# Kernel tuning notes

Measured on AMD Instinct MI355X. Metric: run time of the kernel, lower is better.

## Reference

```python
import jax, jax.numpy as jnp
import numpy as np

B, T, D, NH = 2, 2048, 1024, 32
HD = D // NH  # 32
EPS = 1e-6


def rms_norm(x):
    # normalize over head dim in fp32, cast back
    ms = jnp.mean(x.astype(jnp.float32) ** 2, axis=-1, keepdims=True)
    return x * jax.lax.rsqrt(ms + EPS).astype(x.dtype)


def apply_rope(x, cos, sin):
    d = x.shape[-1] // 2
    x1, x2 = x[..., :d], x[..., d:]
    c = cos[: x.shape[-2], :d]
    s = sin[: x.shape[-2], :d]
    return jnp.concatenate([x1 * c - x2 * s, x2 * c + x1 * s], axis=-1)


def setup_inputs() -> dict:
    key = jax.random.key(0)
    ks = jax.random.split(key, 5)
    sc = 1.0 / np.sqrt(D)
    x = jax.random.normal(ks[0], (B, T, D), jnp.float32)
    Wq = jax.random.normal(ks[1], (D, D), jnp.float32) * sc
    Wk = jax.random.normal(ks[2], (NH * HD, D), jnp.float32) * sc
    Wv = jax.random.normal(ks[3], (NH * HD, D), jnp.float32) * sc
    Wproj = jax.random.normal(ks[4], (D, D), jnp.float32) * sc
    q_gain = jnp.ones((NH,), jnp.float32)  # qk_gain = 1.0
    # real RoPE tables, shape [T, HD//2]
    pos = np.arange(T, dtype=np.float32)
    inv = 1.0 / (10000.0 ** (np.arange(HD // 2, dtype=np.float32) / (HD // 2)))
    ang = pos[:, None] * inv[None, :]
    cos = jnp.asarray(np.cos(ang), jnp.float32)
    sin = jnp.asarray(np.sin(ang), jnp.float32)
    return {"x": x, "Wq": Wq, "Wk": Wk, "Wv": Wv, "Wproj": Wproj,
            "q_gain": q_gain, "cos": cos, "sin": sin}


def reference(x, Wq, Wk, Wv, Wproj, q_gain, cos, sin):
    Bx, Tx, Dx = x.shape
    nh = q_gain.shape[0]
    hd = Dx // nh
    # projections -> [B, H, T, hd]
    q = (x @ Wq.T).reshape(Bx, Tx, nh, hd).transpose(0, 2, 1, 3)
    k = (x @ Wk.T).reshape(Bx, Tx, nh, hd).transpose(0, 2, 1, 3)
    v = (x @ Wv.T).reshape(Bx, Tx, nh, hd).transpose(0, 2, 1, 3)
    q = apply_rope(rms_norm(q), cos, sin) * q_gain[None, :, None, None]
    k = apply_rope(rms_norm(k), cos, sin)
    scale = hd ** (-0.5)
    scores = jnp.einsum('bhqd,bhkd->bhqk', q, k) * scale
    causal = jnp.tril(jnp.ones((Tx, Tx), bool))
    scores = jnp.where(causal, scores, jnp.finfo(scores.dtype).min)
    attn = jax.nn.softmax(scores, axis=-1)
    y = jnp.einsum('bhqk,bhkd->bhqd', attn, v)
    y = y.transpose(0, 2, 1, 3).reshape(Bx, Tx, Dx)
    return y @ Wproj.T
```

## Files before the change

kernel.cpp:

```cpp
#include <hip/hip_runtime.h>

#define DEV __device__ __forceinline__

typedef __bf16 bf16x8 __attribute__((ext_vector_type(8)));
typedef float f32x4 __attribute__((ext_vector_type(4)));
typedef float f32x16 __attribute__((ext_vector_type(16)));
typedef unsigned int u32x2 __attribute__((ext_vector_type(2)));

static constexpr int Tn = 2048;
static constexpr int Dn = 1024;
static constexpr int NHn = 32;
static constexpr int Mn = 2 * Tn;
static constexpr float QSCALE = 0.17677669529663687f * 1.4426950408889634f;

DEV unsigned short f2bf(float f) {
    return __builtin_bit_cast(unsigned short, (__bf16)f);
}

DEV unsigned pkbf(float lo, float hi) {
    unsigned short l = __builtin_bit_cast(unsigned short, (__bf16)lo);
    unsigned short h = __builtin_bit_cast(unsigned short, (__bf16)hi);
    return (unsigned)l | ((unsigned)h << 16);
}

#define GPTR(p) ((const __attribute__((address_space(1))) void*)(p))
#define LPTR(p) ((__attribute__((address_space(3))) void*)(p))

__global__ __launch_bounds__(256) void cast_all(
    const float* __restrict__ x, const float* __restrict__ Wq, const float* __restrict__ Wk,
    const float* __restrict__ Wv, const float* __restrict__ Wp,
    unsigned short* __restrict__ xb, unsigned short* __restrict__ wall) {
    int i = blockIdx.x * 256 + threadIdx.x;
    const float* src;
    ushort4* dst;
    if (i < (1 << 20)) {
        src = x + (size_t)i * 4;
        dst = reinterpret_cast<ushort4*>(xb) + i;
    } else {
        int j = i - (1 << 20);
        int sel = j >> 18, off = j & ((1 << 18) - 1);
        const float* w = (sel == 0) ? Wq : (sel == 1) ? Wk : (sel == 2) ? Wv : Wp;
        src = w + (size_t)off * 4;
        dst = reinterpret_cast<ushort4*>(wall) + ((size_t)sel << 18) + off;
    }
    float4 v = *reinterpret_cast<const float4*>(src);
    ushort4 o;
    o.x = f2bf(v.x); o.y = f2bf(v.y); o.z = f2bf(v.z); o.w = f2bf(v.w);
    *dst = o;
}

__global__ __launch_bounds__(256) void gemm_qkv(
    const unsigned short* __restrict__ A, const unsigned short* __restrict__ Wall,
    unsigned short* __restrict__ Qn, unsigned short* __restrict__ Kn, unsigned short* __restrict__ Vt,
    const float* __restrict__ gain, const float* __restrict__ cosp, const float* __restrict__ sinp) {
    const int z = blockIdx.z;
    const unsigned short* Bm = Wall + (size_t)z * (Dn * Dn);
    const int m0 = blockIdx.x * 128, n0 = blockIdx.y * 128;
    const int tid = threadIdx.x, w = tid >> 6, l = tid & 63;
    const int wm = w & 1, wn = w >> 1, lm = l & 15, quad = l >> 4;

    __shared__ __align__(16) unsigned short As[128 * 32];
    __shared__ __align__(16) unsigned short Bs[128 * 32];

    f32x4 acc[4][4] = {};

    const int r0 = (w * 2 + 0) * 16 + (l >> 2);
    const int r1 = (w * 2 + 1) * 16 + (l >> 2);
    const int c0 = (l & 3) * 8;
    const unsigned short* gA0 = A + (long)(m0 + r0) * Dn + c0;
    const unsigned short* gA1 = A + (long)(m0 + r1) * Dn + c0;
    const unsigned short* gB0 = Bm + (long)(n0 + r0) * Dn + c0;
    const unsigned short* gB1 = Bm + (long)(n0 + r1) * Dn + c0;
    unsigned short* lA0 = As + (w * 2 + 0) * 16 * 32;
    unsigned short* lA1 = As + (w * 2 + 1) * 16 * 32;
    unsigned short* lB0 = Bs + (w * 2 + 0) * 16 * 32;
    unsigned short* lB1 = Bs + (w * 2 + 1) * 16 * 32;

    for (int kk = 0; kk < Dn; kk += 32) {
        __builtin_amdgcn_global_load_lds(GPTR(gA0 + kk), LPTR(lA0), 16, 0, 0);
        __builtin_amdgcn_global_load_lds(GPTR(gA1 + kk), LPTR(lA1), 16, 0, 0);
        __builtin_amdgcn_global_load_lds(GPTR(gB0 + kk), LPTR(lB0), 16, 0, 0);
        __builtin_amdgcn_global_load_lds(GPTR(gB1 + kk), LPTR(lB1), 16, 0, 0);
        __syncthreads();
        bf16x8 af[4], bfv[4];
#pragma unroll
        for (int mt = 0; mt < 4; ++mt)
            af[mt] = __builtin_bit_cast(bf16x8,
                *reinterpret_cast<const uint4*>(As + (wm * 64 + mt * 16 + lm) * 32 + quad * 8));
#pragma unroll
        for (int nt = 0; nt < 4; ++nt)
            bfv[nt] = __builtin_bit_cast(bf16x8,
                *reinterpret_cast<const uint4*>(Bs + (wn * 64 + nt * 16 + lm) * 32 + quad * 8));
#pragma unroll
        for (int mt = 0; mt < 4; ++mt)
#pragma unroll
            for (int nt = 0; nt < 4; ++nt)
                acc[mt][nt] = __builtin_amdgcn_mfma_f32_16x16x32_bf16(af[mt], bfv[nt], acc[mt][nt], 0, 0, 0);
        __syncthreads();
    }

    if (z == 2) {
#pragma unroll
        for (int mt = 0; mt < 4; ++mt) {
            int row0 = m0 + wm * 64 + mt * 16 + quad * 4;
            int b_ = row0 >> 11, t_ = row0 & (Tn - 1);
#pragma unroll
            for (int nt = 0; nt < 4; ++nt) {
                int col = n0 + wn * 64 + nt * 16 + lm;
                int hh = col >> 5, dd = col & 31;
                ushort4 o4;
                o4.x = f2bf(acc[mt][nt][0]); o4.y = f2bf(acc[mt][nt][1]);
                o4.z = f2bf(acc[mt][nt][2]); o4.w = f2bf(acc[mt][nt][3]);
                *reinterpret_cast<ushort4*>(&Vt[((long)(b_ * NHn + hh) * 32 + dd) * Tn + t_]) = o4;
            }
        }
    } else {
        unsigned short* dst = z ? Kn : Qn;
#pragma unroll
        for (int mt = 0; mt < 4; ++mt)
#pragma unroll
            for (int r = 0; r < 4; ++r) {
                int row = m0 + wm * 64 + mt * 16 + quad * 4 + r;
                int b_ = row >> 11, t_ = row & (Tn - 1);
                float c = cosp[t_ * 16 + lm], s = sinp[t_ * 16 + lm];
#pragma unroll
                for (int g = 0; g < 2; ++g) {
                    float x1 = acc[mt][2 * g][r], x2 = acc[mt][2 * g + 1][r];
                    float ssv = x1 * x1 + x2 * x2;
#pragma unroll
                    for (int off = 8; off >= 1; off >>= 1) ssv += __shfl_xor(ssv, off, 16);
                    float rinv = rsqrtf(ssv * (1.0f / 32.0f) + 1e-6f);
                    x1 *= rinv; x2 *= rinv;
                    float o1 = x1 * c - x2 * s;
                    float o2 = x2 * c + x1 * s;
                    int hh = (n0 + wn * 64 + g * 32) >> 5;
                    if (z == 0) { float gs = gain[hh] * QSCALE; o1 *= gs; o2 *= gs; }
                    long base = ((long)(b_ * NHn + hh) * Tn + t_) * 32;
                    dst[base + lm] = f2bf(o1);
                    dst[base + 16 + lm] = f2bf(o2);
                }
            }
    }
}

__global__ __launch_bounds__(256) void gemm_proj(
    const unsigned short* __restrict__ A, const unsigned short* __restrict__ Bm,
    float* __restrict__ C) {
    const int m0 = blockIdx.x * 128, n0 = blockIdx.y * 128;
    const int tid = threadIdx.x, w = tid >> 6, l = tid & 63;
    const int wm = w & 1, wn = w >> 1, lm = l & 15, quad = l >> 4;

    __shared__ __align__(16) unsigned short As[128 * 32];
    __shared__ __align__(16) unsigned short Bs[128 * 32];

    f32x4 acc[4][4] = {};

    const int r0 = (w * 2 + 0) * 16 + (l >> 2);
    const int r1 = (w * 2 + 1) * 16 + (l >> 2);
    const int c0 = (l & 3) * 8;
    const unsigned short* gA0 = A + (long)(m0 + r0) * Dn + c0;
    const unsigned short* gA1 = A + (long)(m0 + r1) * Dn + c0;
    const unsigned short* gB0 = Bm + (long)(n0 + r0) * Dn + c0;
    const unsigned short* gB1 = Bm + (long)(n0 + r1) * Dn + c0;
    unsigned short* lA0 = As + (w * 2 + 0) * 16 * 32;
    unsigned short* lA1 = As + (w * 2 + 1) * 16 * 32;
    unsigned short* lB0 = Bs + (w * 2 + 0) * 16 * 32;
    unsigned short* lB1 = Bs + (w * 2 + 1) * 16 * 32;

    for (int kk = 0; kk < Dn; kk += 32) {
        __builtin_amdgcn_global_load_lds(GPTR(gA0 + kk), LPTR(lA0), 16, 0, 0);
        __builtin_amdgcn_global_load_lds(GPTR(gA1 + kk), LPTR(lA1), 16, 0, 0);
        __builtin_amdgcn_global_load_lds(GPTR(gB0 + kk), LPTR(lB0), 16, 0, 0);
        __builtin_amdgcn_global_load_lds(GPTR(gB1 + kk), LPTR(lB1), 16, 0, 0);
        __syncthreads();
        bf16x8 af[4], bfv[4];
#pragma unroll
        for (int mt = 0; mt < 4; ++mt)
            af[mt] = __builtin_bit_cast(bf16x8,
                *reinterpret_cast<const uint4*>(As + (wm * 64 + mt * 16 + lm) * 32 + quad * 8));
#pragma unroll
        for (int nt = 0; nt < 4; ++nt)
            bfv[nt] = __builtin_bit_cast(bf16x8,
                *reinterpret_cast<const uint4*>(Bs + (wn * 64 + nt * 16 + lm) * 32 + quad * 8));
#pragma unroll
        for (int mt = 0; mt < 4; ++mt)
#pragma unroll
            for (int nt = 0; nt < 4; ++nt)
                acc[mt][nt] = __builtin_amdgcn_mfma_f32_16x16x32_bf16(af[mt], bfv[nt], acc[mt][nt], 0, 0, 0);
        __syncthreads();
    }
#pragma unroll
    for (int mt = 0; mt < 4; ++mt)
#pragma unroll
        for (int nt = 0; nt < 4; ++nt)
#pragma unroll
            for (int r = 0; r < 4; ++r) {
                int rg = m0 + wm * 64 + mt * 16 + quad * 4 + r;
                int cg = n0 + wn * 64 + nt * 16 + lm;
                C[(long)rg * Dn + cg] = acc[mt][nt][r];
            }
}

__global__ __launch_bounds__(256) void attn(
    const unsigned short* __restrict__ Qn, const unsigned short* __restrict__ Kn,
    const unsigned short* __restrict__ Vt, unsigned short* __restrict__ Y) {
    const int bx = blockIdx.x, h = blockIdx.y, b = blockIdx.z;
    const int tid = threadIdx.x, w = tid >> 6, l = tid & 63;
    const int lr = l & 31, hf = l >> 5;
    const long bh = b * NHn + h;
    const unsigned short* Qh = Qn + bh * Tn * 32;
    const unsigned short* Kh = Kn + bh * Tn * 32;
    const unsigned short* Vh = Vt + bh * 32 * Tn;

    __shared__ __align__(16) unsigned short KT[2][2048];
    __shared__ __align__(16) unsigned short VT[2][2048];

    const int k_row = w * 16 + (l >> 2);
    const int k_s = ((l & 3) - (k_row >> 1)) & 3;
    const unsigned short* ksrc = Kh + k_row * 32 + k_s * 8;
    const int v_row = w * 8 + (l >> 3);
    const int v_s = ((l & 7) - v_row) & 7;
    const unsigned short* vsrc = Vh + (long)v_row * Tn + v_s * 8;

    for (int pass = 0; pass < 2; ++pass) {
        const int qb = pass ? (15 - bx) : bx;
        const int q0 = qb * 128 + w * 32;

        bf16x8 qf[2];
        qf[0] = __builtin_bit_cast(bf16x8,
            *reinterpret_cast<const uint4*>(Qh + (q0 + lr) * 32 + hf * 8));
        qf[1] = __builtin_bit_cast(bf16x8,
            *reinterpret_cast<const uint4*>(Qh + (q0 + lr) * 32 + 16 + hf * 8));
        float ss = 0.f;
#pragma unroll
        for (int j = 0; j < 8; ++j) {
            float v0 = (float)qf[0][j], v1 = (float)qf[1][j];
            ss += v0 * v0 + v1 * v1;
        }
        ss += __shfl_xor(ss, 32);
        const float Mv = __builtin_sqrtf(ss * 32.0f);
        f32x16 negC;
#pragma unroll
        for (int i = 0; i < 16; ++i) negC[i] = -Mv;

        float lsum = 0.f;
        f32x16 o = {};

        const int kend = q0 + 31;
        const int ntb = 2 * qb + 2;

        auto stage = [&](int buf, int k0) {
            __builtin_amdgcn_global_load_lds(GPTR(ksrc + k0 * 32), LPTR(&KT[buf][w * 512]), 16, 0, 0);
            __builtin_amdgcn_global_load_lds(GPTR(vsrc + k0), LPTR(&VT[buf][w * 512]), 16, 0, 0);
        };

        auto compute_t = [&](int buf, int k0) {
#pragma unroll
            for (int sub = 0; sub < 2; ++sub) {
                const int ks = k0 + sub * 32;
                if (ks > kend) continue;
                const int krow = sub * 32 + lr;
                const int sl0 = ((0 + hf) + (krow >> 1)) & 3;
                const int sl1 = ((2 + hf) + (krow >> 1)) & 3;
                bf16x8 k0f = __builtin_bit_cast(bf16x8,
                    *reinterpret_cast<const uint4*>(&KT[buf][krow * 32 + sl0 * 8]));
                bf16x8 k1f = __builtin_bit_cast(bf16x8,
                    *reinterpret_cast<const uint4*>(&KT[buf][krow * 32 + sl1 * 8]));
                f32x16 st = __builtin_amdgcn_mfma_f32_32x32x16_bf16(k0f, qf[0], negC, 0, 0, 0);
                st = __builtin_amdgcn_mfma_f32_32x32x16_bf16(k1f, qf[1], st, 0, 0, 0);
                const bool full = (ks + 31) <= q0;
                const int qrow = q0 + lr;
                float p[16];
#pragma unroll
                for (int r = 0; r < 16; ++r) {
                    float pv = __builtin_amdgcn_exp2f(st[r]);
                    if (!full) {
                        int kg = ks + (r & 3) + 8 * (r >> 2) + 4 * hf;
                        pv = (kg <= qrow) ? pv : 0.0f;
                    }
                    p[r] = pv;
                }
                float t0 = (p[0] + p[1]) + (p[2] + p[3]);
                float t1 = (p[4] + p[5]) + (p[6] + p[7]);
                float t2 = (p[8] + p[9]) + (p[10] + p[11]);
                float t3 = (p[12] + p[13]) + (p[14] + p[15]);
                lsum += (t0 + t1) + (t2 + t3);
                unsigned A0 = pkbf(p[0], p[1]), A1 = pkbf(p[2], p[3]);
                unsigned B0 = pkbf(p[4], p[5]), B1 = pkbf(p[6], p[7]);
                unsigned A2 = pkbf(p[8], p[9]), A3 = pkbf(p[10], p[11]);
                unsigned B2 = pkbf(p[12], p[13]), B3 = pkbf(p[14], p[15]);
                u32x2 s0 = __builtin_amdgcn_permlane32_swap(A0, B0, false, false);
                u32x2 s1 = __builtin_amdgcn_permlane32_swap(A1, B1, false, false);
                u32x2 s2 = __builtin_amdgcn_permlane32_swap(A2, B2, false, false);
                u32x2 s3 = __builtin_amdgcn_permlane32_swap(A3, B3, false, false);
                uint4 f0; f0.x = s0[0]; f0.y = s1[0]; f0.z = s0[1]; f0.w = s1[1];
                uint4 f1; f1.x = s2[0]; f1.y = s3[0]; f1.z = s2[1]; f1.w = s3[1];
                const int slv0 = ((sub * 4 + 0 + hf) + lr) & 7;
                const int slv1 = ((sub * 4 + 2 + hf) + lr) & 7;
                bf16x8 v0f = __builtin_bit_cast(bf16x8,
                    *reinterpret_cast<const uint4*>(&VT[buf][lr * 64 + slv0 * 8]));
                bf16x8 v1f = __builtin_bit_cast(bf16x8,
                    *reinterpret_cast<const uint4*>(&VT[buf][lr * 64 + slv1 * 8]));
                o = __builtin_amdgcn_mfma_f32_32x32x16_bf16(
                    __builtin_bit_cast(bf16x8, f0), v0f, o, 0, 0, 0);
                o = __builtin_amdgcn_mfma_f32_32x32x16_bf16(
                    __builtin_bit_cast(bf16x8, f1), v1f, o, 0, 0, 0);
            }
        };

        __syncthreads();
        stage(0, 0);
        int cur = 0;
        for (int ti = 0; ti < ntb; ++ti) {
            __syncthreads();
            if (ti + 1 < ntb) stage(cur ^ 1, (ti + 1) * 64);
            compute_t(cur, ti * 64);
            cur ^= 1;
        }

        lsum += __shfl_xor(lsum, 32);
        const float inv = 1.0f / lsum;
#pragma unroll
        for (int r = 0; r < 16; ++r) {
            int qr = (r & 3) + 8 * (r >> 2) + 4 * hf;
            float invr = __shfl(inv, qr);
            long base = ((long)(b * Tn + q0 + qr) * NHn + h) * 32;
            Y[base + lr] = f2bf(o[r] * invr);
        }
    }
}

extern "C" void kernel_launch(void* const* d_in, const int* in_sizes, int n_in,
                              void* d_out, int out_size, void* d_ws, size_t ws_size,
                              hipStream_t stream) {
    (void)in_sizes; (void)n_in; (void)out_size; (void)ws_size;
    const float* x = (const float*)d_in[0];
    const float* Wq = (const float*)d_in[1];
    const float* Wk = (const float*)d_in[2];
    const float* Wv = (const float*)d_in[3];
    const float* Wp = (const float*)d_in[4];
    const float* gain = (const float*)d_in[5];
    const float* cosp = (const float*)d_in[6];
    const float* sinp = (const float*)d_in[7];

    char* ws = (char*)d_ws;
    const size_t SZ = (size_t)Mn * Dn * 2;
    unsigned short* xb = (unsigned short*)ws;
    unsigned short* wall = (unsigned short*)(ws + SZ);
    unsigned short* qn = (unsigned short*)(ws + 2 * SZ);
    unsigned short* kn = qn + (size_t)Mn * Dn;
    unsigned short* vt = kn + (size_t)Mn * Dn;
    unsigned short* ybuf = vt + (size_t)Mn * Dn;

    cast_all<<<8192, 256, 0, stream>>>(x, Wq, Wk, Wv, Wp, xb, wall);

    gemm_qkv<<<dim3(Mn / 128, Dn / 128, 3), 256, 0, stream>>>(
        xb, wall, qn, kn, vt, gain, cosp, sinp);

    attn<<<dim3(8, NHn, 2), 256, 0, stream>>>(qn, kn, vt, ybuf);

    gemm_proj<<<dim3(Mn / 128, Dn / 128), 256, 0, stream>>>(
        ybuf, wall + (size_t)3 * Dn * Dn, (float*)d_out);
}
```

Before: 227.4 us.

## Split attention KV range across two wave groups and merge partials in LDS

Doubles the attention block to 512 threads. Two groups of four waves each take half of the key tiles for the same query rows, each with its own double-buffered K/V staging. Group 1 writes its partial O accumulator and row sum to LDS, and group 0 adds them and does the normalization and store. This raises parallelism per block and shortens the serial KV loop, at the cost of more LDS, an extra barrier and the partial-merge step. It works without rescaling because a fixed max bound is used instead of an online max.

```diff
diff --git a/kernel.cpp b/kernel.cpp
--- a/kernel.cpp
+++ b/kernel.cpp
@@ -201,30 +201,32 @@
             }
 }
 
-__global__ __launch_bounds__(256) void attn(
+__global__ __launch_bounds__(512) void attn(
     const unsigned short* __restrict__ Qn, const unsigned short* __restrict__ Kn,
     const unsigned short* __restrict__ Vt, unsigned short* __restrict__ Y) {
     const int bx = blockIdx.x, h = blockIdx.y, b = blockIdx.z;
     const int tid = threadIdx.x, w = tid >> 6, l = tid & 63;
+    const int wq = w & 3, kg = w >> 2;
     const int lr = l & 31, hf = l >> 5;
     const long bh = b * NHn + h;
     const unsigned short* Qh = Qn + bh * Tn * 32;
     const unsigned short* Kh = Kn + bh * Tn * 32;
     const unsigned short* Vh = Vt + bh * 32 * Tn;
 
-    __shared__ __align__(16) unsigned short KT[2][2048];
-    __shared__ __align__(16) unsigned short VT[2][2048];
-
-    const int k_row = w * 16 + (l >> 2);
+    __shared__ __align__(16) unsigned short KT[2][2][2048];
+    __shared__ __align__(16) unsigned short VT[2][2][2048];
+    __shared__ float Po[4][64][17];
+
+    const int k_row = wq * 16 + (l >> 2);
     const int k_s = ((l & 3) - (k_row >> 1)) & 3;
     const unsigned short* ksrc = Kh + k_row * 32 + k_s * 8;
-    const int v_row = w * 8 + (l >> 3);
+    const int v_row = wq * 8 + (l >> 3);
     const int v_s = ((l & 7) - v_row) & 7;
     const unsigned short* vsrc = Vh + (long)v_row * Tn + v_s * 8;
 
     for (int pass = 0; pass < 2; ++pass) {
         const int qb = pass ? (15 - bx) : bx;
-        const int q0 = qb * 128 + w * 32;
+        const int q0 = qb * 128 + wq * 32;
 
         bf16x8 qf[2];
         qf[0] = __builtin_bit_cast(bf16x8,
@@ -247,11 +249,12 @@
         f32x16 o = {};
 
         const int kend = q0 + 31;
-        const int ntb = 2 * qb + 2;
-
-        auto stage = [&](int buf, int k0) {
-            __builtin_amdgcn_global_load_lds(GPTR(ksrc + k0 * 32), LPTR(&KT[buf][w * 512]), 16, 0, 0);
-            __builtin_amdgcn_global_load_lds(GPTR(vsrc + k0), LPTR(&VT[buf][w * 512]), 16, 0, 0);
+        const int cnt = qb + 1;
+        const int ts = kg ? cnt : 0;
+
+        auto stage = [&](int buf, int kt) {
+            __builtin_amdgcn_global_load_lds(GPTR(ksrc + kt * 64 * 32), LPTR(&KT[kg][buf][wq * 512]), 16, 0, 0);
+            __builtin_amdgcn_global_load_lds(GPTR(vsrc + kt * 64), LPTR(&VT[kg][buf][wq * 512]), 16, 0, 0);
         };
 
         auto compute_t = [&](int buf, int k0) {
@@ -263,9 +266,9 @@
                 const int sl0 = ((0 + hf) + (krow >> 1)) & 3;
                 const int sl1 = ((2 + hf) + (krow >> 1)) & 3;
                 bf16x8 k0f = __builtin_bit_cast(bf16x8,
-                    *reinterpret_cast<const uint4*>(&KT[buf][krow * 32 + sl0 * 8]));
+                    *reinterpret_cast<const uint4*>(&KT[kg][buf][krow * 32 + sl0 * 8]));
                 bf16x8 k1f = __builtin_bit_cast(bf16x8,
-                    *reinterpret_cast<const uint4*>(&KT[buf][krow * 32 + sl1 * 8]));
+                    *reinterpret_cast<const uint4*>(&KT[kg][buf][krow * 32 + sl1 * 8]));
                 f32x16 st = __builtin_amdgcn_mfma_f32_32x32x16_bf16(k0f, qf[0], negC, 0, 0, 0);
                 st = __builtin_amdgcn_mfma_f32_32x32x16_bf16(k1f, qf[1], st, 0, 0, 0);
                 const bool full = (ks + 31) <= q0;
@@ -275,8 +278,8 @@
                 for (int r = 0; r < 16; ++r) {
                     float pv = __builtin_amdgcn_exp2f(st[r]);
                     if (!full) {
-                        int kg = ks + (r & 3) + 8 * (r >> 2) + 4 * hf;
-                        pv = (kg <= qrow) ? pv : 0.0f;
+                        int kgc = ks + (r & 3) + 8 * (r >> 2) + 4 * hf;
+                        pv = (kgc <= qrow) ? pv : 0.0f;
                     }
                     p[r] = pv;
                 }
@@ -298,9 +301,9 @@
                 const int slv0 = ((sub * 4 + 0 + hf) + lr) & 7;
                 const int slv1 = ((sub * 4 + 2 + hf) + lr) & 7;
                 bf16x8 v0f = __builtin_bit_cast(bf16x8,
-                    *reinterpret_cast<const uint4*>(&VT[buf][lr * 64 + slv0 * 8]));
+                    *reinterpret_cast<const uint4*>(&VT[kg][buf][lr * 64 + slv0 * 8]));
                 bf16x8 v1f = __builtin_bit_cast(bf16x8,
-                    *reinterpret_cast<const uint4*>(&VT[buf][lr * 64 + slv1 * 8]));
+                    *reinterpret_cast<const uint4*>(&VT[kg][buf][lr * 64 + slv1 * 8]));
                 o = __builtin_amdgcn_mfma_f32_32x32x16_bf16(
                     __builtin_bit_cast(bf16x8, f0), v0f, o, 0, 0, 0);
                 o = __builtin_amdgcn_mfma_f32_32x32x16_bf16(
@@ -308,25 +311,36 @@
             }
         };
 
-        __syncthreads();
-        stage(0, 0);
+        stage(0, ts);
         int cur = 0;
-        for (int ti = 0; ti < ntb; ++ti) {
+        for (int i = 0; i < cnt; ++i) {
             __syncthreads();
-            if (ti + 1 < ntb) stage(cur ^ 1, (ti + 1) * 64);
-            compute_t(cur, ti * 64);
+            if (i + 1 < cnt) stage(cur ^ 1, ts + i + 1);
+            compute_t(cur, (ts + i) * 64);
             cur ^= 1;
         }
 
-        lsum += __shfl_xor(lsum, 32);
-        const float inv = 1.0f / lsum;
-#pragma unroll
-        for (int r = 0; r < 16; ++r) {
-            int qr = (r & 3) + 8 * (r >> 2) + 4 * hf;
-            float invr = __shfl(inv, qr);
-            long base = ((long)(b * Tn + q0 + qr) * NHn + h) * 32;
-            Y[base + lr] = f2bf(o[r] * invr);
-        }
+        if (kg) {
+            float* p = &Po[wq][l][0];
+#pragma unroll
+            for (int r = 0; r < 16; ++r) p[r] = o[r];
+            p[16] = lsum;
+        }
+        __syncthreads();
+        if (!kg) {
+            const float* p = &Po[wq][l][0];
+            float ls = lsum + p[16];
+            ls += __shfl_xor(ls, 32);
+            const float inv = 1.0f / ls;
+#pragma unroll
+            for (int r = 0; r < 16; ++r) {
+                int qr = (r & 3) + 8 * (r >> 2) + 4 * hf;
+                float invr = __shfl(inv, qr);
+                long base = ((long)(b * Tn + q0 + qr) * NHn + h) * 32;
+                Y[base + lr] = f2bf((o[r] + p[r]) * invr);
+            }
+        }
+        __syncthreads();
     }
 }
 
@@ -357,7 +371,7 @@
     gemm_qkv<<<dim3(Mn / 128, Dn / 128, 3), 256, 0, stream>>>(
         xb, wall, qn, kn, vt, gain, cosp, sinp);
 
-    attn<<<dim3(8, NHn, 2), 256, 0, stream>>>(qn, kn, vt, ybuf);
+    attn<<<dim3(8, NHn, 2), 512, 0, stream>>>(qn, kn, vt, ybuf);
 
     gemm_proj<<<dim3(Mn / 128, Dn / 128), 256, 0, stream>>>(
         ybuf, wall + (size_t)3 * Dn * Dn, (float*)d_out);
```

Result: no change. 225.8 us (-0.7%).
